# Performance work log

Hardware: AMD Instinct MI355X
Metric: run time of the kernel (lower is better)

## Reference

```python
import jax, jax.numpy as jnp
import numpy as np

N_NODES = 50000
N_EDGES = 200000
IN_DIM = 512
HID = 2000
LAT = 128


def setup_inputs() -> dict:
    key = jax.random.key(0)
    ks = jax.random.split(key, 6)
    x = jax.random.normal(ks[0], (N_NODES, IN_DIM), dtype=jnp.float32)
    edge_index = jax.random.randint(ks[1], (2, N_EDGES), 0, N_NODES, dtype=jnp.int64)
    # glorot-ish scales so ReLU/Sigmoid stay in a sane range
    W1 = jax.random.normal(ks[2], (IN_DIM, HID), dtype=jnp.float32) * (1.0 / np.sqrt(IN_DIM))
    b1 = jnp.zeros((HID,), dtype=jnp.float32)
    W2 = jax.random.normal(ks[3], (HID, LAT), dtype=jnp.float32) * (1.0 / np.sqrt(HID))
    b2 = jnp.zeros((LAT,), dtype=jnp.float32)
    return {"x": x, "edge_index": edge_index, "W1": W1, "b1": b1, "W2": W2, "b2": b2}


def gcn_conv(x, edge_index, W, b):
    """PyG GCNConv: D^-1/2 (A+I) D^-1/2 (X W) + b, unit edge weights."""
    n = x.shape[0]
    loops = jnp.arange(n, dtype=edge_index.dtype)
    row = jnp.concatenate([edge_index[0], loops])  # source nodes
    col = jnp.concatenate([edge_index[1], loops])  # target nodes
    deg = jax.ops.segment_sum(jnp.ones_like(col, dtype=x.dtype), col, num_segments=n)
    dis = jnp.where(deg > 0, jax.lax.rsqrt(deg), 0.0)  # deg^-1/2, inf -> 0
    norm = dis[row] * dis[col]                         # [E+N]
    h = x @ W                                          # transform first: [N, out]
    msg = h[row] * norm[:, None]                       # gather + normalize: [E+N, out]
    out = jax.ops.segment_sum(msg, col, num_segments=n)  # scatter-add
    return out + b


def reference(x, edge_index, W1, b1, W2, b2):
    h = jax.nn.relu(gcn_conv(x, edge_index, W1, b1))
    return jax.nn.sigmoid(gcn_conv(h, edge_index, W2, b2))
```

## Files before the change

kernel.cpp:

```cpp
#include <hip/hip_runtime.h>
#include <hip/hip_fp16.h>

#define NN 50000
#define NE 200000
#define IND 512
#define HIDD 2000
#define LATD 128

#define M_PAD 50176
#define N1_PAD 2048
#define MT1 392
#define NBLK 196

typedef _Float16 f16x8 __attribute__((ext_vector_type(8)));
typedef float f32x4 __attribute__((ext_vector_type(4)));

__device__ __forceinline__ void gload_lds16(const _Float16* g, _Float16* l) {
    __builtin_amdgcn_global_load_lds(
        (const __attribute__((address_space(1))) unsigned int*)g,
        (__attribute__((address_space(3))) unsigned int*)l,
        16, 0, 0);
}

__global__ void k_degree(const int* __restrict__ col, int* __restrict__ deg) {
    int e = blockIdx.x * 256 + threadIdx.x;
    if (e < NE) atomicAdd(&deg[col[e]], 1);
}

__global__ void k_dis(const int* __restrict__ deg, float* __restrict__ dis) {
    int i = blockIdx.x * 256 + threadIdx.x;
    if (i < NN) dis[i] = rsqrtf((float)deg[i] + 1.0f);
}

__global__ void k_bsum(const int* __restrict__ deg, int* __restrict__ bsum) {
    __shared__ int sm[4];
    int i = blockIdx.x * 256 + threadIdx.x;
    int v = (i < NN) ? deg[i] : 0;
    #pragma unroll
    for (int off = 32; off; off >>= 1) v += __shfl_down(v, off, 64);
    if ((threadIdx.x & 63) == 0) sm[threadIdx.x >> 6] = v;
    __syncthreads();
    if (threadIdx.x == 0) bsum[blockIdx.x] = sm[0] + sm[1] + sm[2] + sm[3];
}

__global__ void k_bscan(int* __restrict__ bsum) {
    __shared__ int sm[256];
    int tid = threadIdx.x;
    int v = (tid < NBLK) ? bsum[tid] : 0;
    sm[tid] = v;
    __syncthreads();
    #pragma unroll
    for (int off = 1; off < 256; off <<= 1) {
        int t = (tid >= off) ? sm[tid - off] : 0;
        __syncthreads();
        sm[tid] += t;
        __syncthreads();
    }
    if (tid < NBLK) bsum[tid] = sm[tid] - v;
}

__global__ void k_scan_final(const int* __restrict__ deg, const int* __restrict__ bsum,
                             int* __restrict__ row_ptr) {
    __shared__ int sm[256];
    int b = blockIdx.x, tid = threadIdx.x;
    int i = b * 256 + tid;
    int v = (i < NN) ? deg[i] : 0;
    sm[tid] = v;
    __syncthreads();
    #pragma unroll
    for (int off = 1; off < 256; off <<= 1) {
        int t = (tid >= off) ? sm[tid - off] : 0;
        __syncthreads();
        sm[tid] += t;
        __syncthreads();
    }
    if (i < NN) row_ptr[i] = bsum[b] + sm[tid] - v;
    if (i == NN - 1) row_ptr[NN] = bsum[b] + sm[tid];
}

__global__ void k_fill(const int* __restrict__ ei, const int* __restrict__ row_ptr,
                       int* __restrict__ cursor, int* __restrict__ csr_src) {
    int e = blockIdx.x * 256 + threadIdx.x;
    if (e < NE) {
        int r = ei[e], c = ei[NE + e];
        int pos = atomicAdd(&cursor[c], 1);
        csr_src[row_ptr[c] + pos] = r;
    }
}

__global__ void k_transpose_tiled(const float* __restrict__ in,
                                  _Float16* __restrict__ out, int R, int C, int ldo) {
    __shared__ float sm[32][33];
    int c0 = blockIdx.x * 32, r0 = blockIdx.y * 32;
    int tx = threadIdx.x & 31, ty = threadIdx.x >> 5;
    #pragma unroll
    for (int i = 0; i < 4; ++i) {
        int r = r0 + ty + i * 8, c = c0 + tx;
        sm[ty + i * 8][tx] = (r < R && c < C) ? in[(size_t)r * C + c] : 0.f;
    }
    __syncthreads();
    #pragma unroll
    for (int i = 0; i < 4; ++i) {
        int c = c0 + ty + i * 8, r = r0 + tx;
        if (c < C && r < R) out[(size_t)c * ldo + r] = (_Float16)sm[tx][ty + i * 8];
    }
}

__global__ void k_xcvt(const float* __restrict__ in, _Float16* __restrict__ out, int n8) {
    int i = blockIdx.x * 256 + threadIdx.x;
    if (i < n8) {
        float4 a = ((const float4*)in)[i * 2];
        float4 b = ((const float4*)in)[i * 2 + 1];
        f16x8 o;
        o[0] = (_Float16)a.x; o[1] = (_Float16)a.y; o[2] = (_Float16)a.z; o[3] = (_Float16)a.w;
        o[4] = (_Float16)b.x; o[5] = (_Float16)b.y; o[6] = (_Float16)b.z; o[7] = (_Float16)b.w;
        ((f16x8*)out)[i] = o;
    }
}

__global__ void k_gather_x(const _Float16* __restrict__ xh, const int* __restrict__ row_ptr,
                           const int* __restrict__ csr_src, const float* __restrict__ dis,
                           _Float16* __restrict__ Ah) {
    int dst = blockIdx.x * 4 + (threadIdx.x >> 6);
    if (dst >= NN) return;
    int lane = threadIdx.x & 63;
    float dd = dis[dst];
    const f16x8* vb = (const f16x8*)xh;
    f16x8 sv = vb[(size_t)dst * 64 + lane];
    float acc[8];
    #pragma unroll
    for (int q = 0; q < 8; ++q) acc[q] = dd * (float)sv[q];
    int beg = row_ptr[dst], end = row_ptr[dst + 1];
    for (int c = beg; c < end; c += 64) {
        int n = end - c; if (n > 64) n = 64;
        int li = (lane < n) ? csr_src[c + lane] : 0;
        float lns = (lane < n) ? dis[li] : 0.f;
        for (int j = 0; j < n; j += 4) {
            int j1 = j + 1 < n ? j + 1 : n - 1;
            int j2 = j + 2 < n ? j + 2 : n - 1;
            int j3 = j + 3 < n ? j + 3 : n - 1;
            int s0 = __shfl(li, j),  s1 = __shfl(li, j1);
            int s2 = __shfl(li, j2), s3 = __shfl(li, j3);
            float w0 = __shfl(lns, j);
            float w1 = (j + 1 < n) ? __shfl(lns, j1) : 0.f;
            float w2 = (j + 2 < n) ? __shfl(lns, j2) : 0.f;
            float w3 = (j + 3 < n) ? __shfl(lns, j3) : 0.f;
            f16x8 v0 = vb[(size_t)s0 * 64 + lane];
            f16x8 v1 = vb[(size_t)s1 * 64 + lane];
            f16x8 v2 = vb[(size_t)s2 * 64 + lane];
            f16x8 v3 = vb[(size_t)s3 * 64 + lane];
            #pragma unroll
            for (int q = 0; q < 8; ++q)
                acc[q] += w0 * (float)v0[q] + w1 * (float)v1[q]
                        + w2 * (float)v2[q] + w3 * (float)v3[q];
        }
    }
    f16x8 o;
    #pragma unroll
    for (int q = 0; q < 8; ++q) o[q] = (_Float16)(dd * acc[q]);
    *(f16x8*)(Ah + (size_t)dst * IND + lane * 8) = o;
}

__global__ void k_gather_t(const float* __restrict__ t, const int* __restrict__ row_ptr,
                           const int* __restrict__ csr_src, const float* __restrict__ dis,
                           const float* __restrict__ b2, float* __restrict__ out) {
    int dst = blockIdx.x * 4 + (threadIdx.x >> 6);
    if (dst >= NN) return;
    int lane = threadIdx.x & 63;
    float dd = dis[dst];
    const float2* vb = (const float2*)t;
    float2 td = vb[(size_t)dst * 64 + lane];
    float accx = dd * td.x, accy = dd * td.y;
    int beg = row_ptr[dst], end = row_ptr[dst + 1];
    for (int c = beg; c < end; c += 64) {
        int n = end - c; if (n > 64) n = 64;
        int li = (lane < n) ? csr_src[c + lane] : 0;
        float lns = (lane < n) ? dis[li] : 0.f;
        for (int j = 0; j < n; j += 4) {
            int j1 = j + 1 < n ? j + 1 : n - 1;
            int j2 = j + 2 < n ? j + 2 : n - 1;
            int j3 = j + 3 < n ? j + 3 : n - 1;
            int s0 = __shfl(li, j),  s1 = __shfl(li, j1);
            int s2 = __shfl(li, j2), s3 = __shfl(li, j3);
            float w0 = __shfl(lns, j);
            float w1 = (j + 1 < n) ? __shfl(lns, j1) : 0.f;
            float w2 = (j + 2 < n) ? __shfl(lns, j2) : 0.f;
            float w3 = (j + 3 < n) ? __shfl(lns, j3) : 0.f;
            float2 v0 = vb[(size_t)s0 * 64 + lane];
            float2 v1 = vb[(size_t)s1 * 64 + lane];
            float2 v2 = vb[(size_t)s2 * 64 + lane];
            float2 v3 = vb[(size_t)s3 * 64 + lane];
            accx += w0 * v0.x + w1 * v1.x + w2 * v2.x + w3 * v3.x;
            accy += w0 * v0.y + w1 * v1.y + w2 * v2.y + w3 * v3.y;
        }
    }
    float2 bb = *(const float2*)(b2 + lane * 2);
    float vx = dd * accx + bb.x;
    float vy = dd * accy + bb.y;
    float2 o;
    o.x = 1.0f / (1.0f + __expf(-vx));
    o.y = 1.0f / (1.0f + __expf(-vy));
    *(float2*)(out + (size_t)dst * LATD + lane * 2) = o;
}

__global__ __launch_bounds__(256, 2) void k_gemm1(
    const _Float16* __restrict__ A,
    const _Float16* __restrict__ Bt,
    const float* __restrict__ bias,
    _Float16* __restrict__ Ch,
    int mT0, int slab)
{
    const int b = blockIdx.x;
    const int mT = mT0 + (b & 7) * slab + ((b >> 3) >> 4);
    const int nT = (b >> 3) & 15;
    const int mBase = mT * 128;
    const int nBase = nT * 128;

    __shared__ __align__(16) _Float16 As[2 * 128 * 32];
    __shared__ __align__(16) _Float16 Bs[2 * 128 * 32];

    const int tid = threadIdx.x;
    const int lane = tid & 63;
    const int w = tid >> 6;

    const int srow = w * 32 + (lane >> 2);
    const int scol = (lane & 3) * 8;
    const _Float16* Ag0 = A + (size_t)(mBase + srow) * IND + scol;
    const _Float16* Ag1 = Ag0 + (size_t)16 * IND;
    const _Float16* Bg0 = Bt + (size_t)(nBase + srow) * IND + scol;
    const _Float16* Bg1 = Bg0 + (size_t)16 * IND;

    const int wm = (w >> 1) * 64;
    const int wn = (w & 1) * 64;
    const int lm = lane & 15;
    const int quad = lane >> 4;

    f32x4 acc[4][4];
    #pragma unroll
    for (int i = 0; i < 4; ++i)
        #pragma unroll
        for (int j = 0; j < 4; ++j)
            acc[i][j] = (f32x4){0.f, 0.f, 0.f, 0.f};

    for (int k0 = 0; k0 < IND; k0 += 64) {
        #pragma unroll
        for (int s = 0; s < 2; ++s) {
            gload_lds16(Ag0 + k0 + s * 32, As + s * 4096 + w * 1024);
            gload_lds16(Ag1 + k0 + s * 32, As + s * 4096 + w * 1024 + 512);
            gload_lds16(Bg0 + k0 + s * 32, Bs + s * 4096 + w * 1024);
            gload_lds16(Bg1 + k0 + s * 32, Bs + s * 4096 + w * 1024 + 512);
        }
        __syncthreads();

        #pragma unroll
        for (int s = 0; s < 2; ++s) {
            f16x8 af[4], bfr[4];
            #pragma unroll
            for (int mi = 0; mi < 4; ++mi)
                af[mi] = *(const f16x8*)&As[s * 4096 + (wm + mi * 16 + lm) * 32 + quad * 8];
            #pragma unroll
            for (int ni = 0; ni < 4; ++ni)
                bfr[ni] = *(const f16x8*)&Bs[s * 4096 + (wn + ni * 16 + lm) * 32 + quad * 8];
            #pragma unroll
            for (int mi = 0; mi < 4; ++mi)
                #pragma unroll
                for (int ni = 0; ni < 4; ++ni)
                    acc[mi][ni] = __builtin_amdgcn_mfma_f32_16x16x32_f16(
                        af[mi], bfr[ni], acc[mi][ni], 0, 0, 0);
        }
        __syncthreads();
    }

    #pragma unroll
    for (int mi = 0; mi < 4; ++mi) {
        #pragma unroll
        for (int ni = 0; ni < 4; ++ni) {
            int col = nBase + wn + ni * 16 + lm;
            float bval = bias[col];
            #pragma unroll
            for (int r = 0; r < 4; ++r) {
                int rowg = mBase + wm + mi * 16 + quad * 4 + r;
                float v = fmaxf(acc[mi][ni][r] + bval, 0.f);
                Ch[(size_t)rowg * N1_PAD + col] = (_Float16)v;
            }
        }
    }
}

__global__ __launch_bounds__(256, 2) void k_gemm2(
    const _Float16* __restrict__ A,
    const _Float16* __restrict__ Bt,
    float* __restrict__ Cf)
{
    __shared__ __align__(16) _Float16 As[2 * 64 * 32];
    __shared__ __align__(16) _Float16 Bs[2 * 128 * 32];

    const int tid = threadIdx.x;
    const int lane = tid & 63;
    const int w = tid >> 6;
    const int mBase = blockIdx.x * 64;

    const int srA = w * 16 + (lane >> 2);
    const int srB = w * 32 + (lane >> 2);
    const int scol = (lane & 3) * 8;
    const _Float16* Ag  = A + (size_t)(mBase + srA) * N1_PAD + scol;
    const _Float16* Bg0 = Bt + (size_t)srB * N1_PAD + scol;
    const _Float16* Bg1 = Bg0 + (size_t)16 * N1_PAD;

    const int wm = (w & 1) * 32;
    const int wn = (w >> 1) * 64;
    const int lm = lane & 15;
    const int quad = lane >> 4;

    f32x4 acc[2][4];
    #pragma unroll
    for (int i = 0; i < 2; ++i)
        #pragma unroll
        for (int j = 0; j < 4; ++j)
            acc[i][j] = (f32x4){0.f, 0.f, 0.f, 0.f};

    for (int k0 = 0; k0 < N1_PAD; k0 += 64) {
        #pragma unroll
        for (int s = 0; s < 2; ++s) {
            gload_lds16(Ag + k0 + s * 32, As + s * 2048 + w * 512);
            gload_lds16(Bg0 + k0 + s * 32, Bs + s * 4096 + w * 1024);
            gload_lds16(Bg1 + k0 + s * 32, Bs + s * 4096 + w * 1024 + 512);
        }
        __syncthreads();

        #pragma unroll
        for (int s = 0; s < 2; ++s) {
            f16x8 af[2], bfr[4];
            #pragma unroll
            for (int mi = 0; mi < 2; ++mi)
                af[mi] = *(const f16x8*)&As[s * 2048 + (wm + mi * 16 + lm) * 32 + quad * 8];
            #pragma unroll
            for (int ni = 0; ni < 4; ++ni)
                bfr[ni] = *(const f16x8*)&Bs[s * 4096 + (wn + ni * 16 + lm) * 32 + quad * 8];
            #pragma unroll
            for (int mi = 0; mi < 2; ++mi)
                #pragma unroll
                for (int ni = 0; ni < 4; ++ni)
                    acc[mi][ni] = __builtin_amdgcn_mfma_f32_16x16x32_f16(
                        af[mi], bfr[ni], acc[mi][ni], 0, 0, 0);
        }
        __syncthreads();
    }

    #pragma unroll
    for (int mi = 0; mi < 2; ++mi) {
        #pragma unroll
        for (int ni = 0; ni < 4; ++ni) {
            int col = wn + ni * 16 + lm;
            #pragma unroll
            for (int r = 0; r < 4; ++r) {
                int rowg = mBase + wm + mi * 16 + quad * 4 + r;
                Cf[(size_t)rowg * LATD + col] = acc[mi][ni][r];
            }
        }
    }
}

extern "C" void kernel_launch(void* const* d_in, const int* in_sizes, int n_in,
                              void* d_out, int out_size, void* d_ws, size_t ws_size,
                              hipStream_t stream) {
    const float* x  = (const float*)d_in[0];
    const int* ei   = (const int*)d_in[1];
    const float* W1 = (const float*)d_in[2];
    const float* b1 = (const float*)d_in[3];
    const float* W2 = (const float*)d_in[4];
    const float* b2 = (const float*)d_in[5];
    float* out = (float*)d_out;

    char* p = (char*)d_ws;
    auto alloc = [&](size_t bytes) {
        char* q = p; p += (bytes + 255) & ~(size_t)255; return q;
    };
    int* deg        = (int*)alloc((size_t)NN * 4);
    int* bsum       = (int*)alloc((size_t)NBLK * 4);
    int* row_ptr    = (int*)alloc((size_t)(NN + 1) * 4);
    int* cursor     = (int*)alloc((size_t)NN * 4);
    int* csr_src    = (int*)alloc((size_t)NE * 4);
    float* dis      = (float*)alloc((size_t)NN * 4);
    float* b1pad    = (float*)alloc((size_t)N1_PAD * 4);
    _Float16* W1T   = (_Float16*)alloc((size_t)N1_PAD * IND * 2);
    _Float16* W2T   = (_Float16*)alloc((size_t)LATD * N1_PAD * 2);
    _Float16* xh    = (_Float16*)alloc((size_t)NN * IND * 2);
    _Float16* Ah    = (_Float16*)alloc((size_t)M_PAD * IND * 2);
    _Float16* h     = (_Float16*)alloc((size_t)M_PAD * N1_PAD * 2);
    float* t        = (float*)alloc((size_t)M_PAD * LATD * 4);

    hipMemsetAsync(deg,    0, (size_t)NN * 4, stream);
    hipMemsetAsync(cursor, 0, (size_t)NN * 4, stream);
    hipMemsetAsync(b1pad,  0, (size_t)N1_PAD * 4, stream);
    hipMemsetAsync(W1T,    0, (size_t)N1_PAD * IND * 2, stream);
    hipMemsetAsync(W2T,    0, (size_t)LATD * N1_PAD * 2, stream);
    hipMemcpyAsync(b1pad, b1, (size_t)HIDD * 4, hipMemcpyDeviceToDevice, stream);

    k_degree<<<(NE + 255) / 256, 256, 0, stream>>>(ei + NE, deg);
    k_dis<<<(NN + 255) / 256, 256, 0, stream>>>(deg, dis);
    k_bsum<<<NBLK, 256, 0, stream>>>(deg, bsum);
    k_bscan<<<1, 256, 0, stream>>>(bsum);
    k_scan_final<<<NBLK, 256, 0, stream>>>(deg, bsum, row_ptr);
    k_fill<<<(NE + 255) / 256, 256, 0, stream>>>(ei, row_ptr, cursor, csr_src);

    {
        dim3 gt1((HIDD + 31) / 32, (IND + 31) / 32);
        k_transpose_tiled<<<gt1, 256, 0, stream>>>(W1, W1T, IND, HIDD, IND);
        dim3 gt2((LATD + 31) / 32, (HIDD + 31) / 32);
        k_transpose_tiled<<<gt2, 256, 0, stream>>>(W2, W2T, HIDD, LATD, N1_PAD);
        k_xcvt<<<(NN * IND / 8 + 255) / 256, 256, 0, stream>>>(x, xh, NN * IND / 8);
    }

    k_gather_x<<<(NN + 3) / 4, 256, 0, stream>>>(xh, row_ptr, csr_src, dis, Ah);

    k_gemm1<<<8 * 25 * 16, 256, 0, stream>>>(Ah, W1T, b1pad, h, 0, 25);
    k_gemm1<<<8 * 24 * 16, 256, 0, stream>>>(Ah, W1T, b1pad, h, 200, 24);
    k_gemm2<<<M_PAD / 64, 256, 0, stream>>>(h, W2T, t);

    k_gather_t<<<(NN + 3) / 4, 256, 0, stream>>>(t, row_ptr, csr_src, dis, b2, out);
}
```

Baseline: 503.0 us.

## Double-buffer gemm2 LDS, fuse dis into scan, drop padding memsets, split gemm1

k_gemm2 now double-buffers its LDS tiles, issuing the global-to-LDS loads for the next K slice before computing the current one, which halves the barriers per iteration and overlaps load latency with MFMA work. k_dis is folded into k_scan_final, and the transpose kernels now write zeros into the padded region, so the W1T/W2T memsets, the b1pad buffer and the bias copy go away. gemm1 bias reads are guarded instead. gemm1 is split into four launches instead of two. The tradeoffs are double the LDS use in gemm2, which may reduce occupancy, and two extra launches for gemm1.

Result: no change. 502.4 us (-0.1%).

```diff
diff --git a/kernel.cpp b/kernel.cpp
--- a/kernel.cpp
+++ b/kernel.cpp
@@ -27,11 +27,6 @@
     if (e < NE) atomicAdd(&deg[col[e]], 1);
 }
 
-__global__ void k_dis(const int* __restrict__ deg, float* __restrict__ dis) {
-    int i = blockIdx.x * 256 + threadIdx.x;
-    if (i < NN) dis[i] = rsqrtf((float)deg[i] + 1.0f);
-}
-
 __global__ void k_bsum(const int* __restrict__ deg, int* __restrict__ bsum) {
     __shared__ int sm[4];
     int i = blockIdx.x * 256 + threadIdx.x;
@@ -60,11 +55,12 @@
 }
 
 __global__ void k_scan_final(const int* __restrict__ deg, const int* __restrict__ bsum,
-                             int* __restrict__ row_ptr) {
+                             int* __restrict__ row_ptr, float* __restrict__ dis) {
     __shared__ int sm[256];
     int b = blockIdx.x, tid = threadIdx.x;
     int i = b * 256 + tid;
     int v = (i < NN) ? deg[i] : 0;
+    if (i < NN) dis[i] = rsqrtf((float)v + 1.0f);
     sm[tid] = v;
     __syncthreads();
     #pragma unroll
@@ -89,7 +85,8 @@
 }
 
 __global__ void k_transpose_tiled(const float* __restrict__ in,
-                                  _Float16* __restrict__ out, int R, int C, int ldo) {
+                                  _Float16* __restrict__ out, int R, int C, int ldo,
+                                  int Rpad, int Cpad) {
     __shared__ float sm[32][33];
     int c0 = blockIdx.x * 32, r0 = blockIdx.y * 32;
     int tx = threadIdx.x & 31, ty = threadIdx.x >> 5;
@@ -102,7 +99,7 @@
     #pragma unroll
     for (int i = 0; i < 4; ++i) {
         int c = c0 + ty + i * 8, r = r0 + tx;
-        if (c < C && r < R) out[(size_t)c * ldo + r] = (_Float16)sm[tx][ty + i * 8];
+        if (c < Cpad && r < Rpad) out[(size_t)c * ldo + r] = (_Float16)sm[tx][ty + i * 8];
     }
 }
 
@@ -276,7 +273,7 @@
         #pragma unroll
         for (int ni = 0; ni < 4; ++ni) {
             int col = nBase + wn + ni * 16 + lm;
-            float bval = bias[col];
+            float bval = (col < HIDD) ? bias[col] : 0.f;
             #pragma unroll
             for (int r = 0; r < 4; ++r) {
                 int rowg = mBase + wm + mi * 16 + quad * 4 + r;
@@ -292,8 +289,8 @@
     const _Float16* __restrict__ Bt,
     float* __restrict__ Cf)
 {
-    __shared__ __align__(16) _Float16 As[2 * 64 * 32];
-    __shared__ __align__(16) _Float16 Bs[2 * 128 * 32];
+    __shared__ __align__(16) _Float16 As[2 * 4096];
+    __shared__ __align__(16) _Float16 Bs[2 * 8192];
 
     const int tid = threadIdx.x;
     const int lane = tid & 63;
@@ -319,24 +316,24 @@
         for (int j = 0; j < 4; ++j)
             acc[i][j] = (f32x4){0.f, 0.f, 0.f, 0.f};
 
-    for (int k0 = 0; k0 < N1_PAD; k0 += 64) {
+    auto STAGE = [&](int buf, int k0) {
         #pragma unroll
         for (int s = 0; s < 2; ++s) {
-            gload_lds16(Ag + k0 + s * 32, As + s * 2048 + w * 512);
-            gload_lds16(Bg0 + k0 + s * 32, Bs + s * 4096 + w * 1024);
-            gload_lds16(Bg1 + k0 + s * 32, Bs + s * 4096 + w * 1024 + 512);
-        }
-        __syncthreads();
-
+            gload_lds16(Ag + k0 + s * 32, As + buf * 4096 + s * 2048 + w * 512);
+            gload_lds16(Bg0 + k0 + s * 32, Bs + buf * 8192 + s * 4096 + w * 1024);
+            gload_lds16(Bg1 + k0 + s * 32, Bs + buf * 8192 + s * 4096 + w * 1024 + 512);
+        }
+    };
+    auto COMPUTE = [&](int buf) {
         #pragma unroll
         for (int s = 0; s < 2; ++s) {
             f16x8 af[2], bfr[4];
             #pragma unroll
             for (int mi = 0; mi < 2; ++mi)
-                af[mi] = *(const f16x8*)&As[s * 2048 + (wm + mi * 16 + lm) * 32 + quad * 8];
+                af[mi] = *(const f16x8*)&As[buf * 4096 + s * 2048 + (wm + mi * 16 + lm) * 32 + quad * 8];
             #pragma unroll
             for (int ni = 0; ni < 4; ++ni)
-                bfr[ni] = *(const f16x8*)&Bs[s * 4096 + (wn + ni * 16 + lm) * 32 + quad * 8];
+                bfr[ni] = *(const f16x8*)&Bs[buf * 8192 + s * 4096 + (wn + ni * 16 + lm) * 32 + quad * 8];
             #pragma unroll
             for (int mi = 0; mi < 2; ++mi)
                 #pragma unroll
@@ -344,8 +341,23 @@
                     acc[mi][ni] = __builtin_amdgcn_mfma_f32_16x16x32_f16(
                         af[mi], bfr[ni], acc[mi][ni], 0, 0, 0);
         }
-        __syncthreads();
-    }
+    };
+
+    STAGE(0, 0);
+    __syncthreads();
+    #pragma unroll 1
+    for (int it = 0; it < 15; ++it) {
+        STAGE(1, (2 * it + 1) * 64);
+        COMPUTE(0);
+        __syncthreads();
+        STAGE(0, (2 * it + 2) * 64);
+        COMPUTE(1);
+        __syncthreads();
+    }
+    STAGE(1, 31 * 64);
+    COMPUTE(0);
+    __syncthreads();
+    COMPUTE(1);
 
     #pragma unroll
     for (int mi = 0; mi < 2; ++mi) {
@@ -382,7 +394,6 @@
     int* cursor     = (int*)alloc((size_t)NN * 4);
     int* csr_src    = (int*)alloc((size_t)NE * 4);
     float* dis      = (float*)alloc((size_t)NN * 4);
-    float* b1pad    = (float*)alloc((size_t)N1_PAD * 4);
     _Float16* W1T   = (_Float16*)alloc((size_t)N1_PAD * IND * 2);
     _Float16* W2T   = (_Float16*)alloc((size_t)LATD * N1_PAD * 2);
     _Float16* xh    = (_Float16*)alloc((size_t)NN * IND * 2);
@@ -392,30 +403,27 @@
 
     hipMemsetAsync(deg,    0, (size_t)NN * 4, stream);
     hipMemsetAsync(cursor, 0, (size_t)NN * 4, stream);
-    hipMemsetAsync(b1pad,  0, (size_t)N1_PAD * 4, stream);
-    hipMemsetAsync(W1T,    0, (size_t)N1_PAD * IND * 2, stream);
-    hipMemsetAsync(W2T,    0, (size_t)LATD * N1_PAD * 2, stream);
-    hipMemcpyAsync(b1pad, b1, (size_t)HIDD * 4, hipMemcpyDeviceToDevice, stream);
 
     k_degree<<<(NE + 255) / 256, 256, 0, stream>>>(ei + NE, deg);
-    k_dis<<<(NN + 255) / 256, 256, 0, stream>>>(deg, dis);
     k_bsum<<<NBLK, 256, 0, stream>>>(deg, bsum);
     k_bscan<<<1, 256, 0, stream>>>(bsum);
-    k_scan_final<<<NBLK, 256, 0, stream>>>(deg, bsum, row_ptr);
+    k_scan_final<<<NBLK, 256, 0, stream>>>(deg, bsum, row_ptr, dis);
     k_fill<<<(NE + 255) / 256, 256, 0, stream>>>(ei, row_ptr, cursor, csr_src);
 
     {
-        dim3 gt1((HIDD + 31) / 32, (IND + 31) / 32);
-        k_transpose_tiled<<<gt1, 256, 0, stream>>>(W1, W1T, IND, HIDD, IND);
-        dim3 gt2((LATD + 31) / 32, (HIDD + 31) / 32);
-        k_transpose_tiled<<<gt2, 256, 0, stream>>>(W2, W2T, HIDD, LATD, N1_PAD);
+        dim3 gt1(N1_PAD / 32, IND / 32);
+        k_transpose_tiled<<<gt1, 256, 0, stream>>>(W1, W1T, IND, HIDD, IND, IND, N1_PAD);
+        dim3 gt2(LATD / 32, N1_PAD / 32);
+        k_transpose_tiled<<<gt2, 256, 0, stream>>>(W2, W2T, HIDD, LATD, N1_PAD, N1_PAD, LATD);
         k_xcvt<<<(NN * IND / 8 + 255) / 256, 256, 0, stream>>>(x, xh, NN * IND / 8);
     }
 
     k_gather_x<<<(NN + 3) / 4, 256, 0, stream>>>(xh, row_ptr, csr_src, dis, Ah);
 
-    k_gemm1<<<8 * 25 * 16, 256, 0, stream>>>(Ah, W1T, b1pad, h, 0, 25);
-    k_gemm1<<<8 * 24 * 16, 256, 0, stream>>>(Ah, W1T, b1pad, h, 200, 24);
+    k_gemm1<<<8 * 12 * 16, 256, 0, stream>>>(Ah, W1T, b1, h, 0,   12);
+    k_gemm1<<<8 * 12 * 16, 256, 0, stream>>>(Ah, W1T, b1, h, 96,  12);
+    k_gemm1<<<8 * 12 * 16, 256, 0, stream>>>(Ah, W1T, b1, h, 192, 12);
+    k_gemm1<<<8 * 13 * 16, 256, 0, stream>>>(Ah, W1T, b1, h, 288, 13);
     k_gemm2<<<M_PAD / 64, 256, 0, stream>>>(h, W2T, t);
 
     k_gather_t<<<(NN + 3) / 4, 256, 0, stream>>>(t, row_ptr, csr_src, dis, b2, out);
```
